# Optimization experiments

Measured on AMD Instinct MI355X. Metric: run time of the kernel, lower is better.

Reference implementation:

```python
import jax, jax.numpy as jnp
import numpy as np

B, S, H, V = 2, 2048, 4096, 32000

def setup_inputs() -> dict:
    key = jax.random.key(0)
    k1, k2, k3, k4 = jax.random.split(key, 4)
    return {
        "hidden_states": jax.random.normal(k1, (B, S, H), dtype=jnp.float32),
        "head_weight": jax.random.normal(k2, (V, H), dtype=jnp.float32) * 0.02,
        "labels": jax.random.randint(k3, (B, S), 0, V, dtype=jnp.int64),
        "loss_weight": jax.random.uniform(k4, (B, S), dtype=jnp.float32),
        "grad_accumulation_steps": 1,
    }

def reference(hidden_states, head_weight, labels, loss_weight, grad_accumulation_steps):
    # logits = F.linear(hidden_states, head_weight)  -> [B, S, V]
    logits = jnp.einsum("bsh,vh->bsv", hidden_states, head_weight)
    flat_logits = logits.reshape(-1, logits.shape[-1])   # [T, V]
    flat_labels = labels.reshape(-1)                      # [T]
    # per-token cross entropy (reduction='none'): -log_softmax[label]
    logz = jax.nn.logsumexp(flat_logits, axis=-1)         # [T]
    picked = jnp.take_along_axis(flat_logits, flat_labels[:, None], axis=-1)[:, 0]
    per_tok = logz - picked                               # [T]
    w = loss_weight.reshape(-1)
    w_sum = jnp.sum(w)  # all_reduce(mean) is identity on one device
    loss = jnp.sum(per_tok * w) / (w_sum + 1e-8)
    loss = loss / grad_accumulation_steps
    return loss
```

## Files before the change

### kernel.cpp

```cpp
#include <hip/hip_runtime.h>
#include <hip/hip_bf16.h>

#define T_TOK 4096
#define HDIM  4096
#define VOCAB 32000
#define BM8   256
#define BN8   256
#define BKB   128
#define NT_K  (HDIM / BKB)
#define NTT8  (T_TOK / BM8)
#define NVT8  (VOCAB / BN8)

typedef float f32x4 __attribute__((ext_vector_type(4)));
typedef int   i32x4 __attribute__((ext_vector_type(4)));

#define GLD_LDS16(gsrc, ldst)                                                  \
  __builtin_amdgcn_global_load_lds(                                            \
      (const __attribute__((address_space(1))) void*)(gsrc),                   \
      (__attribute__((address_space(3))) void*)(ldst), 16, 0, 0)

__global__ __launch_bounds__(256) void ce_quant_38766374814398(
    const float* __restrict__ in, signed char* __restrict__ out,
    float* __restrict__ scales)
{
  const int row = blockIdx.x;
  const int tid = threadIdx.x;
  const float* src = in + (size_t)row * HDIM;

  f32x4 v[4];
  float mx = 0.f;
#pragma unroll
  for (int j = 0; j < 4; ++j) {
    v[j] = *(const f32x4*)(src + tid * 16 + j * 4);
    mx = fmaxf(mx, fmaxf(fmaxf(fabsf(v[j][0]), fabsf(v[j][1])),
                         fmaxf(fabsf(v[j][2]), fabsf(v[j][3]))));
  }
#pragma unroll
  for (int off = 1; off < 64; off <<= 1)
    mx = fmaxf(mx, __shfl_xor(mx, off, 64));
  __shared__ float wm4[4];
  if ((tid & 63) == 0) wm4[tid >> 6] = mx;
  __syncthreads();
  mx = fmaxf(fmaxf(wm4[0], wm4[1]), fmaxf(wm4[2], wm4[3]));
  mx = fmaxf(mx, 1e-20f);
  const float inv = 127.0f / mx;
  if (tid == 0) scales[row] = mx / 127.0f;

  i32x4 o;
#pragma unroll
  for (int j = 0; j < 4; ++j) {
    int b0 = min(127, max(-127, __float2int_rn(v[j][0] * inv))) & 0xff;
    int b1 = min(127, max(-127, __float2int_rn(v[j][1] * inv))) & 0xff;
    int b2 = min(127, max(-127, __float2int_rn(v[j][2] * inv))) & 0xff;
    int b3 = min(127, max(-127, __float2int_rn(v[j][3] * inv))) & 0xff;
    o[j] = b0 | (b1 << 8) | (b2 << 16) | (b3 << 24);
  }
  *(i32x4*)(out + (size_t)row * HDIM + tid * 16) = o;
}

__global__ __launch_bounds__(512, 2) void ce_gemm8q_38766374814398(
    const signed char* __restrict__ Aq, const signed char* __restrict__ Wq,
    const float* __restrict__ s_t, const float* __restrict__ s_v,
    const int* __restrict__ labels, float* __restrict__ sumexp,
    float* __restrict__ picked)
{
  __shared__ __attribute__((aligned(16))) signed char sA0[BM8 * BKB];
  __shared__ __attribute__((aligned(16))) signed char sA1[BM8 * BKB];
  __shared__ __attribute__((aligned(16))) signed char sB0[BN8 * BKB];
  __shared__ __attribute__((aligned(16))) signed char sB1[BN8 * BKB];

  const int tid  = threadIdx.x;
  const int lane = tid & 63;
  const int wid  = tid >> 6;
  const int wm   = wid >> 2;
  const int wn   = wid & 3;

  const int bid = blockIdx.x;
  const int tt  = (bid & 7) * 2 + ((bid >> 3) & 1);
  const int vt  = (bid >> 3) >> 1;

  const signed char* gA = Aq + (size_t)tt * BM8 * HDIM;
  const signed char* gB = Wq + (size_t)vt * BN8 * HDIM;

  const int kswB = (((lane & 7) ^ (lane >> 3)) << 4);

#define STAGE_A(arr, kt, half)                                                 \
  do {                                                                         \
    _Pragma("unroll")                                                          \
    for (int call = 0; call < 2; ++call) {                                     \
      const int chunk = call * 16 + (half) * 8 + wid;                          \
      const int row   = chunk * 8 + (lane >> 3);                               \
      GLD_LDS16(gA + (size_t)row * HDIM + (size_t)(kt) * BKB + kswB,           \
                &(arr)[chunk * 1024]);                                         \
    }                                                                          \
  } while (0)

#define STAGE_B(arr, kt, half)                                                 \
  do {                                                                         \
    _Pragma("unroll")                                                          \
    for (int call = 0; call < 2; ++call) {                                     \
      const int chunk = (half) * 16 + call * 8 + wid;                          \
      const int row   = chunk * 8 + (lane >> 3);                               \
      GLD_LDS16(gB + (size_t)row * HDIM + (size_t)(kt) * BKB + kswB,           \
                &(arr)[chunk * 1024]);                                         \
    }                                                                          \
  } while (0)

#define B_READ(arr)                                                            \
  _Pragma("unroll")                                                            \
  for (int ni = 0; ni < 4; ++ni)                                               \
    _Pragma("unroll")                                                          \
    for (int s = 0; s < 2; ++s) {                                              \
      const int br   = wn * 64 + ni * 16 + (lane & 15);                        \
      const int cidx = s * 4 + (lane >> 4);                                    \
      bfrag[ni][s] =                                                           \
          *(const i32x4*)&(arr)[br * BKB + ((cidx ^ (br & 7)) << 4)];          \
    }

#define A_READ_TO(dst, q, arr)                                                 \
  _Pragma("unroll")                                                            \
  for (int mi = 0; mi < 2; ++mi)                                               \
    _Pragma("unroll")                                                          \
    for (int s = 0; s < 2; ++s) {                                              \
      const int ar   = wm * 128 + (q) * 32 + mi * 16 + (lane & 15);            \
      const int cidx = s * 4 + (lane >> 4);                                    \
      dst[mi][s] =                                                             \
          *(const i32x4*)&(arr)[ar * BKB + ((cidx ^ (ar & 7)) << 4)];          \
    }

#define PHASE_SYNC()                                                           \
  do {                                                                         \
    __builtin_amdgcn_sched_barrier(0);                                         \
    __builtin_amdgcn_s_barrier();                                              \
    __builtin_amdgcn_sched_barrier(0);                                         \
  } while (0)

#define DO_MFMA_F(q, FR)                                                       \
  do {                                                                         \
    __builtin_amdgcn_s_setprio(1);                                             \
    _Pragma("unroll")                                                          \
    for (int mi = 0; mi < 2; ++mi)                                             \
      _Pragma("unroll")                                                        \
      for (int ni = 0; ni < 4; ++ni)                                           \
        _Pragma("unroll")                                                      \
        for (int s = 0; s < 2; ++s)                                            \
          acc[(q) * 2 + mi][ni] = __builtin_amdgcn_mfma_i32_16x16x64_i8(       \
              FR[mi][s], bfrag[ni][s], acc[(q) * 2 + mi][ni], 0, 0, 0);        \
    __builtin_amdgcn_s_setprio(0);                                             \
  } while (0)

#define TILE(t, CA, CB, OA, OB)                                                \
  do {                                                                         \
    i32x4 bfrag[4][2];                                                         \
    i32x4 afA[2][2];                                                           \
    i32x4 afB[2][2];                                                           \
     \
    B_READ(CB);                                                                \
    A_READ_TO(afA, 0, CA);                                                     \
    A_READ_TO(afB, 1, CA);                                                     \
    if ((t) + 1 < NT_K) STAGE_A(OA, (t) + 1, 1);                               \
    PHASE_SYNC();                                                              \
    DO_MFMA_F(0, afA);                                                         \
    __builtin_amdgcn_sched_barrier(0);                                         \
    __builtin_amdgcn_s_barrier();                                              \
            \
    A_READ_TO(afA, 2, CA);                                                     \
    if ((t) + 2 < NT_K) STAGE_B(CB, (t) + 2, 0);                               \
    PHASE_SYNC();                                                              \
    DO_MFMA_F(1, afB);                                                         \
    __builtin_amdgcn_sched_barrier(0);                                         \
    __builtin_amdgcn_s_barrier();                                              \
                       \
    A_READ_TO(afB, 3, CA);                                                     \
    if ((t) + 2 < NT_K) STAGE_B(CB, (t) + 2, 1);                               \
    PHASE_SYNC();                                                              \
    DO_MFMA_F(2, afA);                                                         \
    __builtin_amdgcn_sched_barrier(0);                                         \
    __builtin_amdgcn_s_barrier();                                              \
          \
    if ((t) + 2 < NT_K) STAGE_A(CA, (t) + 2, 0);                               \
    PHASE_SYNC();                                                              \
    DO_MFMA_F(3, afB);                                                         \
    __builtin_amdgcn_sched_barrier(0);                                         \
    if ((t) + 2 < NT_K)      asm volatile("s_waitcnt vmcnt(6)" ::: "memory");  \
    else if ((t) + 1 < NT_K) asm volatile("s_waitcnt vmcnt(0)" ::: "memory");  \
    __builtin_amdgcn_s_barrier();                                              \
  } while (0)

  i32x4 acc[8][4];
#pragma unroll
  for (int i = 0; i < 8; ++i)
#pragma unroll
    for (int j = 0; j < 4; ++j)
      acc[i][j] = (i32x4){0, 0, 0, 0};

  STAGE_B(sB0, 0, 0);
  STAGE_B(sB0, 0, 1);
  STAGE_A(sA0, 0, 0);
  STAGE_A(sA0, 0, 1);
  asm volatile("s_waitcnt vmcnt(4)" ::: "memory");
  STAGE_B(sB1, 1, 0);
  STAGE_B(sB1, 1, 1);
  STAGE_A(sA1, 1, 0);
  asm volatile("s_waitcnt vmcnt(6)" ::: "memory");
  __builtin_amdgcn_s_barrier();

  for (int t = 0; t < NT_K; t += 2) {
    TILE(t,     sA0, sB0, sA1, sB1);
    TILE(t + 1, sA1, sB1, sA0, sB0);
  }

  const int row0 = tt * BM8 + wm * 128 + ((lane >> 4) << 2);
  const int col0 = vt * BN8 + wn * 64 + (lane & 15);
  float sv[4];
#pragma unroll
  for (int ni = 0; ni < 4; ++ni) sv[ni] = s_v[col0 + ni * 16];
#pragma unroll
  for (int mi = 0; mi < 8; ++mi) {
#pragma unroll
    for (int r = 0; r < 4; ++r) {
      const int row = row0 + mi * 16 + r;
      const int lab = labels[row];
      const float st = s_t[row];
      float se = 0.f;
#pragma unroll
      for (int ni = 0; ni < 4; ++ni) {
        const float lg = (float)acc[mi][ni][r] * st * sv[ni];
        se += expf(lg);
        if (col0 + ni * 16 == lab) picked[row] = lg;
      }
      se += __shfl_xor(se, 1, 64);
      se += __shfl_xor(se, 2, 64);
      se += __shfl_xor(se, 4, 64);
      se += __shfl_xor(se, 8, 64);
      if ((lane & 15) == 0) atomicAdd(&sumexp[row], se);
    }
  }
#undef STAGE_A
#undef STAGE_B
#undef B_READ
#undef A_READ_TO
#undef PHASE_SYNC
#undef DO_MFMA_F
#undef TILE
}

typedef __bf16 bf16x8 __attribute__((ext_vector_type(8)));
#define BM 128
#define BN 128
#define BK 64
#define NTT (T_TOK / BM)
#define NVT (VOCAB / BN)
__global__ __launch_bounds__(256) void ce_fused_gemm_38766374814398(
    const float* __restrict__ hs, const float* __restrict__ wt,
    const int* __restrict__ labels, float* __restrict__ sumexp,
    float* __restrict__ picked)
{
  __shared__ __bf16 lA[BM * BK];
  __shared__ __bf16 lB[BN * BK];

  const int tid  = threadIdx.x;
  const int lane = tid & 63;
  const int wid  = tid >> 6;
  const int wm   = wid >> 1;
  const int wn   = wid & 1;

  const int bid = blockIdx.x;
  const int sw  = (bid & 7) * (NTT * NVT / 8) + (bid >> 3);
  const int vt  = sw >> 5;
  const int tt  = sw & 31;

  const float* gA = hs + (size_t)tt * BM * HDIM;
  const float* gB = wt + (size_t)vt * BN * HDIM;

  f32x4 acc[4][4];
#pragma unroll
  for (int i = 0; i < 4; ++i)
#pragma unroll
    for (int j = 0; j < 4; ++j)
      acc[i][j] = (f32x4){0.f, 0.f, 0.f, 0.f};

  for (int kt = 0; kt < HDIM / BK; ++kt) {
    const int kbase = kt * BK;
#pragma unroll
    for (int t = 0; t < 4; ++t) {
      const int c   = t * 256 + tid;
      const int row = c >> 3;
      const int kc  = (c & 7) << 3;
      const float* g = gA + (size_t)row * HDIM + kbase + kc;
      f32x4 p0 = *(const f32x4*)g;
      f32x4 p1 = *(const f32x4*)(g + 4);
      bf16x8 v;
      v[0] = (__bf16)p0[0]; v[1] = (__bf16)p0[1]; v[2] = (__bf16)p0[2]; v[3] = (__bf16)p0[3];
      v[4] = (__bf16)p1[0]; v[5] = (__bf16)p1[1]; v[6] = (__bf16)p1[2]; v[7] = (__bf16)p1[3];
      *(bf16x8*)&lA[(row << 6) + ((((c & 7) ^ row) & 7) << 3)] = v;
    }
#pragma unroll
    for (int t = 0; t < 4; ++t) {
      const int c   = t * 256 + tid;
      const int row = c >> 3;
      const int kc  = (c & 7) << 3;
      const float* g = gB + (size_t)row * HDIM + kbase + kc;
      f32x4 p0 = *(const f32x4*)g;
      f32x4 p1 = *(const f32x4*)(g + 4);
      bf16x8 v;
      v[0] = (__bf16)p0[0]; v[1] = (__bf16)p0[1]; v[2] = (__bf16)p0[2]; v[3] = (__bf16)p0[3];
      v[4] = (__bf16)p1[0]; v[5] = (__bf16)p1[1]; v[6] = (__bf16)p1[2]; v[7] = (__bf16)p1[3];
      *(bf16x8*)&lB[(row << 6) + ((((c & 7) ^ row) & 7) << 3)] = v;
    }
    __syncthreads();

#pragma unroll
    for (int kk = 0; kk < 2; ++kk) {
      bf16x8 af[4], bfr[4];
      const int slot = kk * 4 + (lane >> 4);
#pragma unroll
      for (int mi = 0; mi < 4; ++mi) {
        const int ar = wm * 64 + mi * 16 + (lane & 15);
        af[mi] = *(const bf16x8*)&lA[(ar << 6) + (((slot ^ ar) & 7) << 3)];
      }
#pragma unroll
      for (int ni = 0; ni < 4; ++ni) {
        const int br = wn * 64 + ni * 16 + (lane & 15);
        bfr[ni] = *(const bf16x8*)&lB[(br << 6) + (((slot ^ br) & 7) << 3)];
      }
#pragma unroll
      for (int mi = 0; mi < 4; ++mi)
#pragma unroll
        for (int ni = 0; ni < 4; ++ni)
          acc[mi][ni] = __builtin_amdgcn_mfma_f32_16x16x32_bf16(af[mi], bfr[ni], acc[mi][ni], 0, 0, 0);
    }
    __syncthreads();
  }

  const int row0 = tt * BM + wm * 64 + ((lane >> 4) << 2);
  const int col0 = vt * BN + wn * 64 + (lane & 15);
#pragma unroll
  for (int mi = 0; mi < 4; ++mi) {
#pragma unroll
    for (int r = 0; r < 4; ++r) {
      const int row = row0 + mi * 16 + r;
      const int lab = labels[row];
      float se = 0.f;
#pragma unroll
      for (int ni = 0; ni < 4; ++ni) {
        const float lg = acc[mi][ni][r];
        se += expf(lg);
        if (col0 + ni * 16 == lab) picked[row] = lg;
      }
      se += __shfl_xor(se, 1, 64);
      se += __shfl_xor(se, 2, 64);
      se += __shfl_xor(se, 4, 64);
      se += __shfl_xor(se, 8, 64);
      if ((lane & 15) == 0) atomicAdd(&sumexp[row], se);
    }
  }
}

__global__ __launch_bounds__(256) void ce_reduce_38766374814398(
    const float* __restrict__ sumexp, const float* __restrict__ picked,
    const float* __restrict__ lw, const int* __restrict__ gas,
    float* __restrict__ out)
{
  __shared__ float sl[4], sww[4];
  const int tid = threadIdx.x;
  float accl = 0.f, accw = 0.f;
  for (int t = tid; t < T_TOK; t += 256) {
    const float w = lw[t];
    accl += w * (logf(sumexp[t]) - picked[t]);
    accw += w;
  }
#pragma unroll
  for (int off = 32; off > 0; off >>= 1) {
    accl += __shfl_down(accl, off, 64);
    accw += __shfl_down(accw, off, 64);
  }
  if ((tid & 63) == 0) { sl[tid >> 6] = accl; sww[tid >> 6] = accw; }
  __syncthreads();
  if (tid == 0) {
    float L = 0.f, W = 0.f;
#pragma unroll
    for (int i = 0; i < 4; ++i) { L += sl[i]; W += sww[i]; }
    out[0] = L / (W + 1e-8f) / (float)gas[0];
  }
}

extern "C" void kernel_launch(void* const* d_in, const int* in_sizes, int n_in,
                              void* d_out, int out_size, void* d_ws, size_t ws_size,
                              hipStream_t stream) {
  const float* hs     = (const float*)d_in[0];
  const float* wt     = (const float*)d_in[1];
  const int*   labels = (const int*)d_in[2];
  const float* lw     = (const float*)d_in[3];
  const int*   gas    = (const int*)d_in[4];

  const size_t off_sumexp = 0;
  const size_t off_picked = 16384;
  const size_t off_st     = 32768;
  const size_t off_sv     = 49152;
  const size_t off_hq     = 177152;
  const size_t off_wq     = 177152 + (size_t)T_TOK * HDIM;
  const size_t need       = off_wq + (size_t)VOCAB * HDIM;

  float* sumexp = (float*)((char*)d_ws + off_sumexp);
  float* picked = (float*)((char*)d_ws + off_picked);

  hipMemsetAsync(sumexp, 0, T_TOK * sizeof(float), stream);

  if (ws_size >= need) {
    float* s_t = (float*)((char*)d_ws + off_st);
    float* s_v = (float*)((char*)d_ws + off_sv);
    signed char* hq = (signed char*)d_ws + off_hq;
    signed char* wq = (signed char*)d_ws + off_wq;

    ce_quant_38766374814398<<<dim3(T_TOK), dim3(256), 0, stream>>>(hs, hq, s_t);
    ce_quant_38766374814398<<<dim3(VOCAB), dim3(256), 0, stream>>>(wt, wq, s_v);
    ce_gemm8q_38766374814398<<<dim3(NTT8 * NVT8), dim3(512), 0, stream>>>(
        hq, wq, s_t, s_v, labels, sumexp, picked);
  } else {
    ce_fused_gemm_38766374814398<<<dim3(NTT * NVT), dim3(256), 0, stream>>>(
        hs, wt, labels, sumexp, picked);
  }
  ce_reduce_38766374814398<<<dim3(1), dim3(256), 0, stream>>>(
      sumexp, picked, lw, gas, (float*)d_out);
}
```

Before: 748.0 us.

## Collapse int8 GEMM K-tile pipeline from four phases to two half-tile phases

```diff
diff --git a/kernel.cpp b/kernel.cpp
--- a/kernel.cpp
+++ b/kernel.cpp
@@ -117,14 +117,14 @@
           *(const i32x4*)&(arr)[br * BKB + ((cidx ^ (br & 7)) << 4)];          \
     }
 
-#define A_READ_TO(dst, q, arr)                                                 \
+#define A_READ_H(dst, h, arr)                                                  \
   _Pragma("unroll")                                                            \
-  for (int mi = 0; mi < 2; ++mi)                                               \
+  for (int b = 0; b < 4; ++b)                                                  \
     _Pragma("unroll")                                                          \
     for (int s = 0; s < 2; ++s) {                                              \
-      const int ar   = wm * 128 + (q) * 32 + mi * 16 + (lane & 15);            \
+      const int ar   = wm * 128 + (h) * 64 + b * 16 + (lane & 15);             \
       const int cidx = s * 4 + (lane >> 4);                                    \
-      dst[mi][s] =                                                             \
+      dst[b][s] =                                                              \
           *(const i32x4*)&(arr)[ar * BKB + ((cidx ^ (ar & 7)) << 4)];          \
     }
 
@@ -135,52 +135,41 @@
     __builtin_amdgcn_sched_barrier(0);                                         \
   } while (0)
 
-#define DO_MFMA_F(q, FR)                                                       \
+#define DO_MFMA_H(h, FR)                                                       \
   do {                                                                         \
     __builtin_amdgcn_s_setprio(1);                                             \
     _Pragma("unroll")                                                          \
-    for (int mi = 0; mi < 2; ++mi)                                             \
+    for (int b = 0; b < 4; ++b)                                                \
       _Pragma("unroll")                                                        \
       for (int ni = 0; ni < 4; ++ni)                                           \
         _Pragma("unroll")                                                      \
         for (int s = 0; s < 2; ++s)                                            \
-          acc[(q) * 2 + mi][ni] = __builtin_amdgcn_mfma_i32_16x16x64_i8(       \
-              FR[mi][s], bfrag[ni][s], acc[(q) * 2 + mi][ni], 0, 0, 0);        \
+          acc[(h) * 4 + b][ni] = __builtin_amdgcn_mfma_i32_16x16x64_i8(        \
+              FR[b][s], bfrag[ni][s], acc[(h) * 4 + b][ni], 0, 0, 0);          \
     __builtin_amdgcn_s_setprio(0);                                             \
   } while (0)
 
-#define TILE(t, CA, CB, OA, OB)                                                \
+#define TILE(t, CA, CB, OA)                                                    \
   do {                                                                         \
     i32x4 bfrag[4][2];                                                         \
-    i32x4 afA[2][2];                                                           \
-    i32x4 afB[2][2];                                                           \
-     \
+    i32x4 aq[4][2];                                                            \
+              \
     B_READ(CB);                                                                \
-    A_READ_TO(afA, 0, CA);                                                     \
-    A_READ_TO(afB, 1, CA);                                                     \
+    A_READ_H(aq, 0, CA);                                                       \
     if ((t) + 1 < NT_K) STAGE_A(OA, (t) + 1, 1);                               \
     PHASE_SYNC();                                                              \
-    DO_MFMA_F(0, afA);                                                         \
+    DO_MFMA_H(0, aq);                                                          \
     __builtin_amdgcn_sched_barrier(0);                                         \
     __builtin_amdgcn_s_barrier();                                              \
-            \
-    A_READ_TO(afA, 2, CA);                                                     \
-    if ((t) + 2 < NT_K) STAGE_B(CB, (t) + 2, 0);                               \
+      \
+    A_READ_H(aq, 1, CA);                                                       \
+    if ((t) + 2 < NT_K) {                                                      \
+      STAGE_B(CB, (t) + 2, 0);                                                 \
+      STAGE_B(CB, (t) + 2, 1);                                                 \
+      STAGE_A(CA, (t) + 2, 0);                                                 \
+    }                                                                          \
     PHASE_SYNC();                                                              \
-    DO_MFMA_F(1, afB);                                                         \
-    __builtin_amdgcn_sched_barrier(0);                                         \
-    __builtin_amdgcn_s_barrier();                                              \
-                       \
-    A_READ_TO(afB, 3, CA);                                                     \
-    if ((t) + 2 < NT_K) STAGE_B(CB, (t) + 2, 1);                               \
-    PHASE_SYNC();                                                              \
-    DO_MFMA_F(2, afA);                                                         \
-    __builtin_amdgcn_sched_barrier(0);                                         \
-    __builtin_amdgcn_s_barrier();                                              \
-          \
-    if ((t) + 2 < NT_K) STAGE_A(CA, (t) + 2, 0);                               \
-    PHASE_SYNC();                                                              \
-    DO_MFMA_F(3, afB);                                                         \
+    DO_MFMA_H(1, aq);                                                          \
     __builtin_amdgcn_sched_barrier(0);                                         \
     if ((t) + 2 < NT_K)      asm volatile("s_waitcnt vmcnt(6)" ::: "memory");  \
     else if ((t) + 1 < NT_K) asm volatile("s_waitcnt vmcnt(0)" ::: "memory");  \
@@ -198,7 +187,6 @@
   STAGE_B(sB0, 0, 1);
   STAGE_A(sA0, 0, 0);
   STAGE_A(sA0, 0, 1);
-  asm volatile("s_waitcnt vmcnt(4)" ::: "memory");
   STAGE_B(sB1, 1, 0);
   STAGE_B(sB1, 1, 1);
   STAGE_A(sA1, 1, 0);
@@ -206,8 +194,8 @@
   __builtin_amdgcn_s_barrier();
 
   for (int t = 0; t < NT_K; t += 2) {
-    TILE(t,     sA0, sB0, sA1, sB1);
-    TILE(t + 1, sA1, sB1, sA0, sB0);
+    TILE(t,     sA0, sB0, sA1);
+    TILE(t + 1, sA1, sB1, sA0);
   }
 
   const int row0 = tt * BM8 + wm * 128 + ((lane >> 4) << 2);
@@ -239,9 +227,9 @@
 #undef STAGE_A
 #undef STAGE_B
 #undef B_READ
-#undef A_READ_TO
+#undef A_READ_H
 #undef PHASE_SYNC
-#undef DO_MFMA_F
+#undef DO_MFMA_H
 #undef TILE
 }
 
```

After: 804.4 us. +7.5%, slower.
